# Kernel optimization log

Measured on AMD Instinct MI355X. Metric: run time of the kernel, lower is better.

## Reference

```python
import jax, jax.numpy as jnp
import numpy as np

N_NODES = 75000
N_EDGES = 1200000


def gcn_conv(x, src, dst, W, b, n):
    # linear transform first (PyG GCNConv applies lin before propagate)
    h = x @ W  # [n, out]
    # add self loops
    loop = jnp.arange(n, dtype=src.dtype)
    s = jnp.concatenate([src, loop])
    d = jnp.concatenate([dst, loop])
    # symmetric normalization: deg computed on destination after self-loops
    deg = jnp.zeros((n,), dtype=h.dtype).at[d].add(1.0)
    dinv = jnp.where(deg > 0, jax.lax.rsqrt(deg), 0.0)
    norm = dinv[s] * dinv[d]  # [E+n]
    msgs = h[s] * norm[:, None]  # gather + scale, [E+n, out]
    out = jax.ops.segment_sum(msgs, d, num_segments=n)  # scatter-add
    return out + b


def setup_inputs() -> dict:
    key = jax.random.key(0)
    ks = jax.random.split(key, 6)
    x = jax.random.normal(ks[0], (N_NODES, 64), dtype=jnp.float32)
    edge_index = jax.random.randint(ks[1], (2, N_EDGES), 0, N_NODES, dtype=jnp.int64)
    # Glorot-ish scaled weights
    W1 = jax.random.normal(ks[2], (64, 64), dtype=jnp.float32) * (1.0 / np.sqrt(64))
    b1 = jax.random.normal(ks[3], (64,), dtype=jnp.float32) * 0.01
    W2 = jax.random.normal(ks[4], (64, 16), dtype=jnp.float32) * (1.0 / np.sqrt(64))
    b2 = jax.random.normal(ks[5], (16,), dtype=jnp.float32) * 0.01
    return {"x": x, "edge_index": edge_index, "W1": W1, "b1": b1, "W2": W2, "b2": b2}


def reference(x, edge_index, W1, b1, W2, b2):
    src, dst = edge_index[0], edge_index[1]
    h = gcn_conv(x, src, dst, W1, b1, N_NODES)
    h = jax.nn.relu(h)
    # dropout is identity in eval mode
    out = gcn_conv(h, src, dst, W2, b2, N_NODES)
    return out
```

## Files before the change

### kernel.cpp

```cpp
#include <hip/hip_runtime.h>


#define NBSHIFT 9
#define BUCKET_NODES 512
#define CAP 10240
#define CHA 8192
#define TA 512
#define TB 512
#define MAXNB 160

__global__ void kA_zero(int* __restrict__ bucketCur, int NB) {
  int i = blockIdx.x * blockDim.x + threadIdx.x;
  if (i < NB) bucketCur[i] = 0;
}

__launch_bounds__(TA)
__global__ void kA_bucket(const int* __restrict__ src, const int* __restrict__ dst,
                          int* __restrict__ bucketCur, int* __restrict__ bucketArr,
                          int NB, int E) {
  __shared__ int stage[CHA];
  __shared__ unsigned char binOf[CHA];
  __shared__ int cnt[MAXNB];
  __shared__ int off[MAXNB];
  __shared__ int gpos[MAXNB];
  __shared__ int cursor[MAXNB];
  __shared__ int scanbuf[256];
  int t = threadIdx.x;
  int e0 = blockIdx.x * CHA;

  for (int i = t; i < NB; i += TA) cnt[i] = 0;
  __syncthreads();
  for (int i = t; i < CHA; i += TA) {
    int e = e0 + i;
    if (e < E) atomicAdd(&cnt[dst[e] >> NBSHIFT], 1);
  }
  __syncthreads();
  if (t < 256) scanbuf[t] = (t < NB) ? cnt[t] : 0;
  __syncthreads();
  for (int o = 1; o < 256; o <<= 1) {
    int add = (t < 256 && t >= o) ? scanbuf[t - o] : 0;
    __syncthreads();
    if (t < 256) scanbuf[t] += add;
    __syncthreads();
  }
  if (t < NB) {
    off[t] = scanbuf[t] - cnt[t];
    cursor[t] = off[t];
    gpos[t] = (cnt[t] > 0) ? atomicAdd(&bucketCur[t], cnt[t]) : 0;
  }
  __syncthreads();
  for (int i = t; i < CHA; i += TA) {
    int e = e0 + i;
    if (e < E) {
      int d = dst[e], s = src[e];
      int b = d >> NBSHIFT;
      int p = atomicAdd(&cursor[b], 1);
      stage[p] = (s << NBSHIFT) | (d & (BUCKET_NODES - 1));
      binOf[p] = (unsigned char)b;
    }
  }
  __syncthreads();
  int total = scanbuf[255];
  for (int i = t; i < total; i += TA) {
    int b = binOf[i];
    int destIdx = gpos[b] + (i - off[b]);
    if (destIdx < CAP) bucketArr[b * CAP + destIdx] = stage[i];
  }
}

__global__ void kB_scan(const int* __restrict__ bucketCur, int* __restrict__ bucketBase,
                        int* __restrict__ rp, int NB, int N) {
  __shared__ int s[256];
  int t = threadIdx.x;
  int v = (t < NB) ? min(bucketCur[t], CAP) : 0;
  s[t] = v;
  __syncthreads();
  for (int o = 1; o < 256; o <<= 1) {
    int add = (t >= o) ? s[t - o] : 0;
    __syncthreads();
    s[t] += add;
    __syncthreads();
  }
  if (t < NB) bucketBase[t] = s[t] - v;
  if (t == NB - 1) {
    bucketBase[NB] = s[t];
    rp[N] = s[t];
  }
}

__launch_bounds__(TB)
__global__ void kB_fill(const int* __restrict__ bucketArr, const int* __restrict__ bucketCur,
                        const int* __restrict__ bucketBase,
                        int* __restrict__ rp, float* __restrict__ dinv,
                        int* __restrict__ col, int N) {
  __shared__ int hist[BUCKET_NODES];
  __shared__ int noff[BUCKET_NODES];
  __shared__ int cur[BUCKET_NODES];
  __shared__ int colStage[CAP];
  int b = blockIdx.x;
  int t = threadIdx.x;
  int nE = min(bucketCur[b], CAP);
  int base = b * CAP;

  hist[t] = 0;
  __syncthreads();
  for (int i = t; i < nE; i += TB) {
    atomicAdd(&hist[bucketArr[base + i] & (BUCKET_NODES - 1)], 1);
  }
  __syncthreads();
  int myv = hist[t];
  noff[t] = myv;
  __syncthreads();
  for (int o = 1; o < BUCKET_NODES; o <<= 1) {
    int add = (t >= o) ? noff[t - o] : 0;
    __syncthreads();
    noff[t] += add;
    __syncthreads();
  }
  int excl = noff[t] - myv;
  cur[t] = excl;
  int gnode = b * BUCKET_NODES + t;
  if (gnode < N) {
    rp[gnode] = bucketBase[b] + excl;
    dinv[gnode] = rsqrtf((float)(myv + 1));
  }
  __syncthreads();
  for (int i = t; i < nE; i += TB) {
    int v = bucketArr[base + i];
    int p = atomicAdd(&cur[v & (BUCKET_NODES - 1)], 1);
    colStage[p] = v >> NBSHIFT;
  }
  __syncthreads();
  int gb = bucketBase[b];
  for (int i = t; i < nE; i += TB) col[gb + i] = colStage[i];
}

__launch_bounds__(256)
__global__ void k_gemm64(const float4* __restrict__ X4, const float4* __restrict__ W4,
                         const float* __restrict__ dinv, float4* __restrict__ out4,
                         int n) {
  __shared__ float4 Xs[64 * 17];
  __shared__ float4 Ws[64 * 16];
  int t = threadIdx.x;
  int base = blockIdx.x * 64;
  {
    int rr = t >> 2, q = t & 3;
    int r = base + rr;
    #pragma unroll
    for (int c = 0; c < 4; c++) {
      float4 v = make_float4(0.f, 0.f, 0.f, 0.f);
      if (r < n) v = X4[r * 16 + q * 4 + c];
      Xs[rr * 17 + q * 4 + c] = v;
      Ws[t + 256 * c] = W4[t + 256 * c];
    }
  }
  __syncthreads();

  int tx = t & 15, ty = t >> 4;
  float4 a0 = make_float4(0.f, 0.f, 0.f, 0.f), a1 = a0, a2 = a0, a3 = a0;
  #pragma unroll
  for (int kb = 0; kb < 16; kb++) {
    float4 x0 = Xs[(ty * 4 + 0) * 17 + kb];
    float4 x1 = Xs[(ty * 4 + 1) * 17 + kb];
    float4 x2 = Xs[(ty * 4 + 2) * 17 + kb];
    float4 x3 = Xs[(ty * 4 + 3) * 17 + kb];
    float4 w0 = Ws[(kb * 4 + 0) * 16 + tx];
    float4 w1 = Ws[(kb * 4 + 1) * 16 + tx];
    float4 w2 = Ws[(kb * 4 + 2) * 16 + tx];
    float4 w3 = Ws[(kb * 4 + 3) * 16 + tx];
    #define FMA4(A, XS) \
      A.x = fmaf(XS.x, w0.x, A.x); A.y = fmaf(XS.x, w0.y, A.y); \
      A.z = fmaf(XS.x, w0.z, A.z); A.w = fmaf(XS.x, w0.w, A.w); \
      A.x = fmaf(XS.y, w1.x, A.x); A.y = fmaf(XS.y, w1.y, A.y); \
      A.z = fmaf(XS.y, w1.z, A.z); A.w = fmaf(XS.y, w1.w, A.w); \
      A.x = fmaf(XS.z, w2.x, A.x); A.y = fmaf(XS.z, w2.y, A.y); \
      A.z = fmaf(XS.z, w2.z, A.z); A.w = fmaf(XS.z, w2.w, A.w); \
      A.x = fmaf(XS.w, w3.x, A.x); A.y = fmaf(XS.w, w3.y, A.y); \
      A.z = fmaf(XS.w, w3.z, A.z); A.w = fmaf(XS.w, w3.w, A.w);
    FMA4(a0, x0) FMA4(a1, x1) FMA4(a2, x2) FMA4(a3, x3)
    #undef FMA4
  }
  #pragma unroll
  for (int i = 0; i < 4; i++) {
    int r = base + ty * 4 + i;
    if (r < n) {
      float s = dinv[r];
      float4 a = (i == 0) ? a0 : (i == 1) ? a1 : (i == 2) ? a2 : a3;
      a.x *= s; a.y *= s; a.z *= s; a.w *= s;
      out4[r * 16 + tx] = a;
    }
  }
}

__launch_bounds__(256)
__global__ void k_agg64_w2(const float4* __restrict__ hs4,
                           const int* __restrict__ rp,
                           const int* __restrict__ col,
                           const float* __restrict__ dinv,
                           const float* __restrict__ b1,
                           const float* __restrict__ W2,
                           float* __restrict__ hs2,
                           int n) {
  int lane = threadIdx.x & 63;
  int c = lane & 15;
  int sub = lane >> 4;
  int node = (blockIdx.x * blockDim.x + threadIdx.x) >> 6;
  if (node >= n) return;

  float4 b14 = ((const float4*)b1)[c];
  float w2r[16];
  #pragma unroll
  for (int i = 0; i < 16; i++) w2r[i] = W2[(sub * 16 + i) * 16 + c];

  int s0 = rp[node], s1 = rp[node + 1];
  int dt = s1 - s0 + 1;
  float ax = 0.f, ay = 0.f, az = 0.f, aw = 0.f;
  int t = sub;
  int idx = 0;
  if (t < dt) idx = (t == 0) ? node : col[s0 + t - 1];
  while (t < dt) {
    int curi = idx;
    int tn = t + 4;
    if (tn < dt) idx = col[s0 + tn - 1];
    float4 row = hs4[curi * 16 + c];
    ax += row.x; ay += row.y; az += row.z; aw += row.w;
    t = tn;
  }
  #pragma unroll
  for (int m = 16; m <= 32; m <<= 1) {
    ax += __shfl_xor(ax, m);
    ay += __shfl_xor(ay, m);
    az += __shfl_xor(az, m);
    aw += __shfl_xor(aw, m);
  }
  float dv = dinv[node];
  float hx = fmaxf(ax * dv + b14.x, 0.f);
  float hy = fmaxf(ay * dv + b14.y, 0.f);
  float hz = fmaxf(az * dv + b14.z, 0.f);
  float hw = fmaxf(aw * dv + b14.w, 0.f);

  float part = 0.f;
  #pragma unroll
  for (int i = 0; i < 16; i++) {
    int srcLane = 4 * sub + (i >> 2);
    float h;
    if ((i & 3) == 0)      h = __shfl(hx, srcLane);
    else if ((i & 3) == 1) h = __shfl(hy, srcLane);
    else if ((i & 3) == 2) h = __shfl(hz, srcLane);
    else                   h = __shfl(hw, srcLane);
    part = fmaf(h, w2r[i], part);
  }
  #pragma unroll
  for (int m = 16; m <= 32; m <<= 1) part += __shfl_xor(part, m);
  if (sub == 0) hs2[node * 16 + c] = part * dv;
}

__launch_bounds__(256)
__global__ void k_agg16(const float4* __restrict__ hs2_4,
                        const int* __restrict__ rp,
                        const int* __restrict__ col,
                        const float* __restrict__ dinv,
                        const float* __restrict__ b2,
                        float4* __restrict__ out4,
                        int n) {
  int lane = threadIdx.x & 63;
  int c = lane & 3;
  int sub = lane >> 2;
  int node = (blockIdx.x * blockDim.x + threadIdx.x) >> 6;
  if (node >= n) return;

  int s0 = rp[node], s1 = rp[node + 1];
  int dt = s1 - s0 + 1;
  float ax = 0.f, ay = 0.f, az = 0.f, aw = 0.f;
  int t = sub;
  int idx = 0;
  if (t < dt) idx = (t == 0) ? node : col[s0 + t - 1];
  while (t < dt) {
    int curi = idx;
    int tn = t + 16;
    if (tn < dt) idx = col[s0 + tn - 1];
    float4 row = hs2_4[curi * 4 + c];
    ax += row.x; ay += row.y; az += row.z; aw += row.w;
    t = tn;
  }
  #pragma unroll
  for (int m = 4; m <= 32; m <<= 1) {
    ax += __shfl_xor(ax, m);
    ay += __shfl_xor(ay, m);
    az += __shfl_xor(az, m);
    aw += __shfl_xor(aw, m);
  }
  if (sub == 0) {
    float dv = dinv[node];
    float4 b24 = ((const float4*)b2)[c];
    float4 o;
    o.x = ax * dv + b24.x;
    o.y = ay * dv + b24.y;
    o.z = az * dv + b24.z;
    o.w = aw * dv + b24.w;
    out4[node * 4 + c] = o;
  }
}

extern "C" void kernel_launch(void* const* d_in, const int* in_sizes, int n_in,
                              void* d_out, int out_size, void* d_ws, size_t ws_size,
                              hipStream_t stream) {
  const float* x  = (const float*)d_in[0];
  const int* edges = (const int*)d_in[1];
  const float* W1 = (const float*)d_in[2];
  const float* b1 = (const float*)d_in[3];
  const float* W2 = (const float*)d_in[4];
  const float* b2 = (const float*)d_in[5];
  float* out = (float*)d_out;

  const int N = in_sizes[0] / 64;
  const int E = in_sizes[1] / 2;
  const int* src = edges;
  const int* dst = edges + E;
  const int NB = (N + BUCKET_NODES - 1) >> NBSHIFT;

  auto align = [](size_t v) { return (v + 255) & ~(size_t)255; };
  char* p = (char*)d_ws;
  float* dinv       = (float*)p; p += align((size_t)N * 4);
  int*   rp         = (int*)p;   p += align((size_t)(N + 1) * 4);
  int*   bucketCur  = (int*)p;   p += align((size_t)MAXNB * 4);
  int*   bucketBase = (int*)p;   p += align((size_t)(MAXNB + 1) * 4);
  int*   col        = (int*)p;   p += align((size_t)E * 4);
  float* hs1        = (float*)p; p += align((size_t)N * 64 * 4);
  float* hs2        = (float*)p; p += align((size_t)N * 16 * 4);
  int* bucketArr = (int*)hs1;

  const int nbA = (E + CHA - 1) / CHA;
  const int nbWave = ((size_t)N * 64 + 255) / 256;

  kA_zero  <<<(NB + 255) / 256, 256, 0, stream>>>(bucketCur, NB);
  kA_bucket<<<nbA, TA, 0, stream>>>(src, dst, bucketCur, bucketArr, NB, E);
  kB_scan  <<<1, 256, 0, stream>>>(bucketCur, bucketBase, rp, NB, N);
  kB_fill  <<<NB, TB, 0, stream>>>(bucketArr, bucketCur, bucketBase, rp, dinv, col, N);

  k_gemm64  <<<(N + 63) / 64, 256, 0, stream>>>((const float4*)x, (const float4*)W1,
                                                dinv, (float4*)hs1, N);
  k_agg64_w2<<<nbWave, 256, 0, stream>>>((const float4*)hs1, rp, col, dinv,
                                         b1, W2, hs2, N);
  k_agg16   <<<nbWave, 256, 0, stream>>>((const float4*)hs2, rp, col, dinv,
                                         b2, (float4*)out, N);
}
```

Measured before the change: 140.9 us.

## Store layer-1 hidden features as bf16 and unroll gather loop by two

The GEMM epilogue now packs the dinv-scaled hidden features into bf16 pairs, halving the intermediate buffer that the first aggregation gathers per edge. The aggregation kernel unpacks bf16 to float and handles two neighbours per loop iteration, with two prefetched column indices, so more loads are in flight. This cuts gather bandwidth in the memory-bound layer-1 aggregation at the cost of bf16 rounding error in the intermediate features.

```diff
diff --git a/kernel.cpp b/kernel.cpp
--- a/kernel.cpp
+++ b/kernel.cpp
@@ -8,6 +8,13 @@
 #define TA 512
 #define TB 512
 #define MAXNB 160
+
+__device__ __forceinline__ unsigned bfpack(float a, float b) {
+  unsigned ua = __float_as_uint(a), ub = __float_as_uint(b);
+  ua += 0x7fffu + ((ua >> 16) & 1u);
+  ub += 0x7fffu + ((ub >> 16) & 1u);
+  return (ua >> 16) | (ub & 0xffff0000u);
+}
 
 __global__ void kA_zero(int* __restrict__ bucketCur, int NB) {
   int i = blockIdx.x * blockDim.x + threadIdx.x;
@@ -137,7 +144,7 @@
 
 __launch_bounds__(256)
 __global__ void k_gemm64(const float4* __restrict__ X4, const float4* __restrict__ W4,
-                         const float* __restrict__ dinv, float4* __restrict__ out4,
+                         const float* __restrict__ dinv, uint2* __restrict__ outb,
                          int n) {
   __shared__ float4 Xs[64 * 17];
   __shared__ float4 Ws[64 * 16];
@@ -186,14 +193,16 @@
     if (r < n) {
       float s = dinv[r];
       float4 a = (i == 0) ? a0 : (i == 1) ? a1 : (i == 2) ? a2 : a3;
-      a.x *= s; a.y *= s; a.z *= s; a.w *= s;
-      out4[r * 16 + tx] = a;
+      uint2 pk;
+      pk.x = bfpack(a.x * s, a.y * s);
+      pk.y = bfpack(a.z * s, a.w * s);
+      outb[r * 16 + tx] = pk;
     }
   }
 }
 
 __launch_bounds__(256)
-__global__ void k_agg64_w2(const float4* __restrict__ hs4,
+__global__ void k_agg64_w2(const uint2* __restrict__ hsb,
                            const int* __restrict__ rp,
                            const int* __restrict__ col,
                            const float* __restrict__ dinv,
@@ -216,14 +225,27 @@
   int dt = s1 - s0 + 1;
   float ax = 0.f, ay = 0.f, az = 0.f, aw = 0.f;
   int t = sub;
-  int idx = 0;
-  if (t < dt) idx = (t == 0) ? node : col[s0 + t - 1];
+  int idx0 = 0, idx1 = 0;
+  if (t < dt)     idx0 = (t == 0) ? node : col[s0 + t - 1];
+  if (t + 4 < dt) idx1 = col[s0 + t + 3];
   while (t < dt) {
-    int curi = idx;
-    int tn = t + 4;
-    if (tn < dt) idx = col[s0 + tn - 1];
-    float4 row = hs4[curi * 16 + c];
-    ax += row.x; ay += row.y; az += row.z; aw += row.w;
+    int cur0 = idx0, cur1 = idx1;
+    bool has1 = (t + 4) < dt;
+    int tn = t + 8;
+    if (tn < dt)     idx0 = col[s0 + tn - 1];
+    if (tn + 4 < dt) idx1 = col[s0 + tn + 3];
+    uint2 u0 = hsb[cur0 * 16 + c];
+    if (has1) {
+      uint2 u1 = hsb[cur1 * 16 + c];
+      ax += __uint_as_float(u1.x << 16);
+      ay += __uint_as_float(u1.x & 0xffff0000u);
+      az += __uint_as_float(u1.y << 16);
+      aw += __uint_as_float(u1.y & 0xffff0000u);
+    }
+    ax += __uint_as_float(u0.x << 16);
+    ay += __uint_as_float(u0.x & 0xffff0000u);
+    az += __uint_as_float(u0.y << 16);
+    aw += __uint_as_float(u0.y & 0xffff0000u);
     t = tn;
   }
   #pragma unroll
@@ -339,8 +361,8 @@
   kB_fill  <<<NB, TB, 0, stream>>>(bucketArr, bucketCur, bucketBase, rp, dinv, col, N);
 
   k_gemm64  <<<(N + 63) / 64, 256, 0, stream>>>((const float4*)x, (const float4*)W1,
-                                                dinv, (float4*)hs1, N);
-  k_agg64_w2<<<nbWave, 256, 0, stream>>>((const float4*)hs1, rp, col, dinv,
+                                                dinv, (uint2*)hs1, N);
+  k_agg64_w2<<<nbWave, 256, 0, stream>>>((const uint2*)hs1, rp, col, dinv,
                                          b1, W2, hs2, N);
   k_agg16   <<<nbWave, 256, 0, stream>>>((const float4*)hs2, rp, col, dinv,
                                          b2, (float4*)out, N);
```

After: 133.4 us. -5.3%, faster.
